# Optimization experiments

Measured on AMD Instinct MI355X. Metric: run time of the kernel, lower is better.

## Reference

```python
import jax, jax.numpy as jnp
import numpy as np

N = 50000      # nodes
E = 800000     # edges (before self-loops)
HD = 256       # hidden_dim
H = 4          # heads
C = 64         # per-head channels (hidden_dim // 4)
L = 3          # num_layers
G = 512        # graphs in batch
NEG = 0.2      # LeakyReLU negative slope
EPS = 1e-5     # BatchNorm eps


def setup_inputs() -> dict:
    key = jax.random.key(0)
    ks = jax.random.split(key, 16)
    s_in = 1.0 / np.sqrt(HD)
    inp = {
        "x": jax.random.normal(ks[0], (N, 9), dtype=jnp.float32),
        "edge_index": jax.random.randint(ks[1], (2, E), 0, N, dtype=jnp.int64),
        "edge_attr": jax.random.normal(ks[2], (E, 5), dtype=jnp.float32),
        "batch": jnp.sort(jax.random.randint(ks[3], (N,), 0, G, dtype=jnp.int64)),
        # embeddings
        "Wn": jax.random.normal(ks[4], (9, HD), dtype=jnp.float32) / 3.0,
        "bn_b": jnp.zeros((HD,), jnp.float32),
        "We": jax.random.normal(ks[5], (5, HD), dtype=jnp.float32) / 2.3,
        "be_b": jnp.zeros((HD,), jnp.float32),
        # per-layer GATConv params (stacked over L)
        "lin_w": jax.random.normal(ks[6], (L, HD, H * C), dtype=jnp.float32) * s_in,
        "att_src": jax.random.normal(ks[7], (L, H, C), dtype=jnp.float32) * s_in,
        "att_dst": jax.random.normal(ks[8], (L, H, C), dtype=jnp.float32) * s_in,
        "lin_edge_w": jax.random.normal(ks[9], (L, HD, H * C), dtype=jnp.float32) * s_in,
        "att_edge": jax.random.normal(ks[10], (L, H, C), dtype=jnp.float32) * s_in,
        "conv_bias": jnp.zeros((L, H * C), jnp.float32),
        # BatchNorm affine params (eval mode: running_mean=0, running_var=1)
        "gamma": jnp.ones((L, HD), jnp.float32),
        "beta": jnp.zeros((L, HD), jnp.float32),
    }
    return inp


def _segment_softmax(logits, seg, num):
    m = jax.ops.segment_max(logits, seg, num_segments=num)
    m = jnp.where(jnp.isfinite(m), m, 0.0)
    e = jnp.exp(logits - m[seg])
    s = jax.ops.segment_sum(e, seg, num_segments=num)
    return e / (s[seg] + 1e-16)


def _gat_layer(x, row, col, edge_attr, lin_w, att_s, att_d, lin_e_w, att_e, bias):
    # add self-loops; self-loop edge_attr = mean of incoming edge_attr (PyG fill_value='mean')
    deg = jax.ops.segment_sum(jnp.ones((row.shape[0],), x.dtype), col, num_segments=N)
    loop_attr = jax.ops.segment_sum(edge_attr, col, num_segments=N) / jnp.maximum(deg, 1.0)[:, None]
    sl = jnp.arange(N, dtype=row.dtype)
    r = jnp.concatenate([row, sl])
    c = jnp.concatenate([col, sl])
    ea = jnp.concatenate([edge_attr, loop_attr], axis=0)  # [E+N, HD]

    xh = (x @ lin_w).reshape(N, H, C)                     # [N,H,C]
    a_src = jnp.einsum('nhc,hc->nh', xh, att_s)           # [N,H]
    a_dst = jnp.einsum('nhc,hc->nh', xh, att_d)
    eh = (ea @ lin_e_w).reshape(-1, H, C)                 # [E+N,H,C]
    a_e = jnp.einsum('ehc,hc->eh', eh, att_e)

    alpha = a_src[r] + a_dst[c] + a_e                     # [E+N,H]
    alpha = jnp.where(alpha >= 0, alpha, NEG * alpha)     # leaky_relu
    alpha = _segment_softmax(alpha, c, N)

    msg = xh[r] * alpha[:, :, None]                       # gather + weight
    out = jax.ops.segment_sum(msg, c, num_segments=N)     # scatter-add
    return out.reshape(N, H * C) + bias


def reference(x, edge_index, edge_attr, batch, Wn, bn_b, We, be_b,
              lin_w, att_src, att_dst, lin_edge_w, att_edge, conv_bias,
              gamma, beta):
    row, col = edge_index[0], edge_index[1]
    h = x @ Wn + bn_b                     # node embedding [N,HD]
    ea = edge_attr @ We + be_b            # edge embedding [E,HD]
    inv_std = 1.0 / jnp.sqrt(1.0 + EPS)   # BN eval, running stats (0,1)
    for l in range(L):
        h = _gat_layer(h, row, col, ea, lin_w[l], att_src[l], att_dst[l],
                       lin_edge_w[l], att_edge[l], conv_bias[l])
        h = h * inv_std * gamma[l] + beta[l]
        h = jax.nn.relu(h)                # dropout = identity (eval)
    # global mean pool over graphs
    cnt = jax.ops.segment_sum(jnp.ones((N,), h.dtype), batch, num_segments=G)
    pooled = jax.ops.segment_sum(h, batch, num_segments=G) / jnp.maximum(cnt, 1.0)[:, None]
    return pooled
```

## Files before the change

### kernel.cpp

```cpp
#include <hip/hip_runtime.h>
#include <hip/hip_fp16.h>
#include <math.h>

#define HD 256
#define NHEAD 4
#define CH 64
#define NLAYER 3
#define NEG_SLOPE 0.2f

typedef __attribute__((ext_vector_type(8))) _Float16 half8;
typedef __attribute__((ext_vector_type(4))) _Float16 half4v;
typedef __attribute__((ext_vector_type(4))) float float4v;
typedef __attribute__((ext_vector_type(4))) unsigned uint4v;

__global__ __launch_bounds__(256) void embed_count_kernel(
    const float* __restrict__ x, const float* __restrict__ Wn,
    const float* __restrict__ bn_b, _Float16* __restrict__ h, int N,
    const int* __restrict__ col, int* __restrict__ deg, int E,
    int embedBlocks) {
  int tid = threadIdx.x;
  if ((int)blockIdx.x < embedBlocks) {
    int base = blockIdx.x * 8;
    __shared__ float xs[8][9];
    int nn = N - base;
    if (nn > 8) nn = 8;
    if (tid < nn * 9) xs[tid / 9][tid % 9] = x[(size_t)base * 9 + tid];
    __syncthreads();
    float b = bn_b[tid];
    for (int i = 0; i < nn; ++i) {
      float v = b;
#pragma unroll
      for (int k = 0; k < 9; ++k) v += xs[i][k] * Wn[k * HD + tid];
      h[(size_t)(base + i) * HD + tid] = (_Float16)v;
    }
  } else {
    int e = (blockIdx.x - embedBlocks) * 256 + tid;
    if (e < E) atomicAdd(&deg[col[e]], 1);
  }
}

__global__ __launch_bounds__(256) void wc_bfrag_kernel(
    const float* __restrict__ lin_edge_w, const float* __restrict__ att_edge,
    const float* __restrict__ We, const float* __restrict__ be_b,
    float* __restrict__ Wc, float* __restrict__ bc,
    const float* __restrict__ lin_w, _Float16* __restrict__ Bf_hi) {
  int tid = threadIdx.x;
  if (blockIdx.x < 12) {
    int lh = blockIdx.x;
    int l = lh >> 2, hh = lh & 3;
    __shared__ float weff[256];
    int j = tid;
    const float* lw = lin_edge_w + (size_t)l * HD * HD + (size_t)j * HD + hh * CH;
    const float* ae = att_edge + l * HD + hh * CH;
    float s = 0.f;
#pragma unroll 8
    for (int c = 0; c < CH; ++c) s += lw[c] * ae[c];
    weff[j] = s;
    __syncthreads();
    if (j < 5) {
      float acc = 0.f;
      for (int t = 0; t < 256; ++t) acc += We[j * HD + t] * weff[t];
      Wc[j * 12 + lh] = acc;
    } else if (j == 5) {
      float acc = 0.f;
      for (int t = 0; t < 256; ++t) acc += be_b[t] * weff[t];
      bc[lh] = acc;
    }
  } else {
    int bid = (blockIdx.x - 12) * 4 + (tid >> 6);
    int l = bid >> 7;
    int kt = (bid >> 4) & 7, ntg = bid & 15;
    int lane = tid & 63;
    const float* B = lin_w + (size_t)l * HD * HD;
    size_t base = ((size_t)bid * 64 + lane) * 8;
    int k0 = kt * 32 + (lane >> 4) * 8;
    int n = ((ntg >= 8) ? 128 : 0) + (lane & 15) * 8 + (ntg & 7);
#pragma unroll
    for (int j = 0; j < 8; ++j) {
      Bf_hi[base + j] = (_Float16)B[(size_t)(k0 + j) * HD + n];
    }
  }
}

__global__ __launch_bounds__(256) void tile_sums_kernel(
    const int* __restrict__ deg, int* __restrict__ tsum, int N) {
  __shared__ int red[256];
  int i = blockIdx.x * 256 + threadIdx.x;
  red[threadIdx.x] = (i < N) ? deg[i] : 0;
  __syncthreads();
  for (int off = 128; off > 0; off >>= 1) {
    if (threadIdx.x < off) red[threadIdx.x] += red[threadIdx.x + off];
    __syncthreads();
  }
  if (threadIdx.x == 0) tsum[blockIdx.x] = red[0];
}

__global__ __launch_bounds__(64) void scan_tsums_kernel(
    const int* __restrict__ tsum, int* __restrict__ toff, int T) {
  int lane = threadIdx.x;
  int carry = 0;
  for (int base = 0; base < T; base += 64) {
    int i = base + lane;
    int orig = (i < T) ? tsum[i] : 0;
    int v = orig;
#pragma unroll
    for (int off = 1; off < 64; off <<= 1) {
      int t = __shfl_up(v, off, 64);
      if (lane >= off) v += t;
    }
    if (i < T) toff[i] = carry + v - orig;
    carry += __shfl(v, 63, 64);
  }
}

__global__ __launch_bounds__(256) void scan_local_kernel(
    const int* __restrict__ deg, const int* __restrict__ toff,
    int* __restrict__ row_start, int N, int E) {
  __shared__ int buf[256];
  int i = blockIdx.x * 256 + threadIdx.x;
  int v = (i < N) ? deg[i] : 0;
  buf[threadIdx.x] = v;
  __syncthreads();
  for (int off = 1; off < 256; off <<= 1) {
    int t = (threadIdx.x >= off) ? buf[threadIdx.x - off] : 0;
    __syncthreads();
    buf[threadIdx.x] += t;
    __syncthreads();
  }
  if (i < N) row_start[i] = toff[blockIdx.x] + buf[threadIdx.x] - v;
  if (blockIdx.x == 0 && threadIdx.x == 0) row_start[N] = E;
}

__global__ __launch_bounds__(256) void scatter_csr_ae_kernel(
    const int* __restrict__ row, const int* __restrict__ col,
    const float* __restrict__ edge_attr, const int* __restrict__ row_start,
    int* __restrict__ cursor, const float* __restrict__ Wc,
    const float* __restrict__ bc, unsigned* __restrict__ ecsr, int E) {
  __shared__ float sWc[60];
  __shared__ float sbc[12];
  int t = threadIdx.x;
  if (t < 60) sWc[t] = Wc[t];
  if (t < 12) sbc[t] = bc[t];
  __syncthreads();
  int e = blockIdx.x * 256 + t;
  if (e >= E) return;
  int c = col[e];
  int p = atomicAdd(&cursor[c], 1);
  float ea[5];
#pragma unroll
  for (int k = 0; k < 5; ++k) ea[k] = edge_attr[(size_t)e * 5 + k];
  unsigned rec[8];
  rec[0] = (unsigned)row[e];
#pragma unroll
  for (int l = 0; l < NLAYER; ++l) {
    float av[NHEAD];
#pragma unroll
    for (int hh = 0; hh < NHEAD; ++hh) {
      int lh = l * NHEAD + hh;
      float s = sbc[lh];
#pragma unroll
      for (int k = 0; k < 5; ++k) s += ea[k] * sWc[k * 12 + lh];
      av[hh] = s;
    }
    __half2 p0 = __floats2half2_rn(av[0], av[1]);
    __half2 p1 = __floats2half2_rn(av[2], av[3]);
    rec[1 + 2 * l] = *(unsigned*)&p0;
    rec[2 + 2 * l] = *(unsigned*)&p1;
  }
  rec[7] = 0u;
  int slot = row_start[c] + p;
  uint4v* dst = (uint4v*)(ecsr + (size_t)slot * 8);
  uint4v v0 = {rec[0], rec[1], rec[2], rec[3]};
  uint4v v1 = {rec[4], rec[5], rec[6], rec[7]};
  dst[0] = v0;
  dst[1] = v1;
}

__global__ __launch_bounds__(512) void mfma_gemm_fused_kernel(
    const _Float16* __restrict__ A, const _Float16* __restrict__ Bf_hi,
    const float* __restrict__ att_s, const float* __restrict__ att_d,
    __half* __restrict__ xh_h, float* __restrict__ a_src,
    float* __restrict__ a_dst, int N) {
  __shared__ _Float16 sBh[4096];
  const int tid = threadIdx.x;
  const int wave = tid >> 6, lane = tid & 63;
  const int m = lane & 15, quad = lane >> 4;
  const int y = blockIdx.y;
  const int rowbase = blockIdx.x * 128 + wave * 16;
  const int arow = rowbase + m;
  const int arowc = (arow < N) ? arow : (N - 1);

  float4v acc[8];
#pragma unroll
  for (int nt = 0; nt < 8; ++nt) acc[nt] = (float4v){0.f, 0.f, 0.f, 0.f};

  for (int kt = 0; kt < 8; ++kt) {
    __syncthreads();
    {
      const float4* gh = (const float4*)(Bf_hi + ((size_t)kt * 16 + y * 8) * 512);
      ((float4*)sBh)[tid] = gh[tid];
    }
    half8 a = *(const half8*)(A + (size_t)arowc * HD + kt * 32 + quad * 8);
    __syncthreads();
#pragma unroll
    for (int nt = 0; nt < 8; ++nt) {
      half8 bhi = *(const half8*)&sBh[nt * 512 + lane * 8];
      acc[nt] = __builtin_amdgcn_mfma_f32_16x16x32_f16(a, bhi, acc[nt], 0, 0, 0);
    }
  }

  const int hh = y * 2 + (m >> 3);
  const int colbase = y * 128 + m * 8;
  float ats[8], atd[8];
#pragma unroll
  for (int nt = 0; nt < 8; ++nt) {
    ats[nt] = att_s[colbase + nt];
    atd[nt] = att_d[colbase + nt];
  }
  _Float16* xf = (_Float16*)xh_h;
#pragma unroll
  for (int r = 0; r < 4; ++r) {
    int orow = rowbase + quad * 4 + r;
    bool valid = orow < N;
    float ps = 0.f, pd = 0.f;
    half8 h0;
#pragma unroll
    for (int nt = 0; nt < 8; ++nt) {
      h0[nt] = (_Float16)acc[nt][r];
      ps += acc[nt][r] * ats[nt];
      pd += acc[nt][r] * atd[nt];
    }
    if (valid) {
      *(half8*)(xf + (size_t)orow * HD + colbase) = h0;
    }
    ps += __shfl_xor(ps, 1, 64);
    ps += __shfl_xor(ps, 2, 64);
    ps += __shfl_xor(ps, 4, 64);
    pd += __shfl_xor(pd, 1, 64);
    pd += __shfl_xor(pd, 2, 64);
    pd += __shfl_xor(pd, 4, 64);
    if (valid && (m & 7) == 0) {
      a_src[(size_t)orow * NHEAD + hh] = ps;
      a_dst[(size_t)orow * NHEAD + hh] = pd;
    }
  }
}

__global__ __launch_bounds__(256) void fused_aggregate_kernel(
    const __half* __restrict__ xh_h, const unsigned* __restrict__ ecsr,
    const int* __restrict__ row_start, int lsel,
    const float* __restrict__ a_src, const float* __restrict__ a_dst,
    const float* __restrict__ cb, const float* __restrict__ gm,
    const float* __restrict__ bt, float inv_std, _Float16* __restrict__ hout,
    int N) {
  int tid = threadIdx.x;
  int n = blockIdx.x * 4 + (tid >> 6);
  if (n >= N) return;
  int lane = tid & 63;
  int s = row_start[n], e = row_start[n + 1];

  const int hw = lane >> 4;
  const int eidx = lane & 15;
  const int t = lane;
  const int ch = t * 4;
  const half4v* xh4 = (const half4v*)xh_h;
  const float based = a_dst[n * 4 + hw];
  const int aofs = 1 + 2 * lsel + (hw >> 1);
  const bool hi_half = (hw & 1);

  float a0 = 0.f, a1 = 0.f, a2 = 0.f, a3 = 0.f;
  float zpart = 0.f, aepart = 0.f;

  const int base_src = lane & 48;
  for (int chunk = s; chunk < e; chunk += 16) {
    int myedge = chunk + eidx;
    int r_my = 0;
    float w_my = 0.f;
    if (myedge < e) {
      const unsigned* rp = ecsr + (size_t)myedge * 8;
      r_my = (int)rp[0];
      unsigned aw = rp[aofs];
      __half2 h2 = *(__half2*)&aw;
      float ae = hi_half ? __high2float(h2) : __low2float(h2);
      float lg = a_src[r_my * 4 + hw] + based + ae;
      lg = (lg >= 0.f) ? lg : NEG_SLOPE * lg;
      w_my = __expf(lg);
      zpart += w_my;
      aepart += ae;
    }
#pragma unroll
    for (int u = 0; u < 16; ++u) {
      float w = __shfl(w_my, base_src + u, 64);
      int ru = __shfl(r_my, base_src + u, 64);
      half4v xv = xh4[(size_t)ru * 64 + t];
      a0 += w * (float)xv[0];
      a1 += w * (float)xv[1];
      a2 += w * (float)xv[2];
      a3 += w * (float)xv[3];
    }
  }
#pragma unroll
  for (int off = 1; off < 16; off <<= 1) {
    zpart += __shfl_xor(zpart, off, 64);
    aepart += __shfl_xor(aepart, off, 64);
  }
  float dinv = (e > s) ? 1.0f / (float)(e - s) : 1.0f;
  float sl = a_src[n * 4 + hw] + based + aepart * dinv;
  sl = (sl >= 0.f) ? sl : NEG_SLOPE * sl;
  float wself = __expf(sl);
  half4v sv = xh4[(size_t)n * 64 + t];
  a0 += wself * (float)sv[0];
  a1 += wself * (float)sv[1];
  a2 += wself * (float)sv[2];
  a3 += wself * (float)sv[3];
  float zinv = 1.0f / (zpart + wself + 1e-16f);

  half4v ho;
  ho[0] = (_Float16)fmaxf((a0 * zinv + cb[ch + 0]) * inv_std * gm[ch + 0] + bt[ch + 0], 0.f);
  ho[1] = (_Float16)fmaxf((a1 * zinv + cb[ch + 1]) * inv_std * gm[ch + 1] + bt[ch + 1], 0.f);
  ho[2] = (_Float16)fmaxf((a2 * zinv + cb[ch + 2]) * inv_std * gm[ch + 2] + bt[ch + 2], 0.f);
  ho[3] = (_Float16)fmaxf((a3 * zinv + cb[ch + 3]) * inv_std * gm[ch + 3] + bt[ch + 3], 0.f);
  *(half4v*)&hout[(size_t)n * HD + ch] = ho;
}

__global__ __launch_bounds__(128) void pool_kernel(
    const _Float16* __restrict__ h, const int* __restrict__ batch,
    float* __restrict__ out, int N) {
  int g = blockIdx.x;
  int ch = blockIdx.y * 128 + threadIdx.x;
  __shared__ int s_lo, s_hi;
  if (threadIdx.x == 0) {
    int lo = 0, hi = N;
    while (lo < hi) { int mid = (lo + hi) >> 1; if (batch[mid] < g) lo = mid + 1; else hi = mid; }
    s_lo = lo;
    lo = 0; hi = N;
    while (lo < hi) { int mid = (lo + hi) >> 1; if (batch[mid] < g + 1) lo = mid + 1; else hi = mid; }
    s_hi = lo;
  }
  __syncthreads();
  int lo = s_lo, hi = s_hi;
  float acc = 0.f;
  for (int n = lo; n < hi; ++n) acc += (float)h[(size_t)n * HD + ch];
  int cnt = hi - lo;
  out[(size_t)g * HD + ch] = acc / (float)(cnt > 0 ? cnt : 1);
}

extern "C" void kernel_launch(void* const* d_in, const int* in_sizes, int n_in,
                              void* d_out, int out_size, void* d_ws, size_t ws_size,
                              hipStream_t stream) {
  const float* x = (const float*)d_in[0];
  const int* ei = (const int*)d_in[1];
  const float* edge_attr = (const float*)d_in[2];
  const int* batch = (const int*)d_in[3];
  const float* Wn = (const float*)d_in[4];
  const float* bn_b = (const float*)d_in[5];
  const float* We = (const float*)d_in[6];
  const float* be_b = (const float*)d_in[7];
  const float* lin_w = (const float*)d_in[8];
  const float* att_src = (const float*)d_in[9];
  const float* att_dst = (const float*)d_in[10];
  const float* lin_edge_w = (const float*)d_in[11];
  const float* att_edge = (const float*)d_in[12];
  const float* conv_bias = (const float*)d_in[13];
  const float* gamma = (const float*)d_in[14];
  const float* beta = (const float*)d_in[15];

  const int N = in_sizes[3];
  const int E = in_sizes[1] / 2;
  const int G = out_size / HD;
  const int* row = ei;
  const int* col = ei + E;

  char* ws = (char*)d_ws;
  size_t off = 0;
  auto alloc = [&](size_t bytes) -> char* {
    char* p = ws + off;
    off += (bytes + 255) & ~(size_t)255;
    return p;
  };
  _Float16* h = (_Float16*)alloc((size_t)N * HD * 2);
  __half* xh_h = (__half*)alloc((size_t)N * HD * 2);
  float* a_src = (float*)alloc((size_t)N * NHEAD * 4);
  float* a_dst = (float*)alloc((size_t)N * NHEAD * 4);
  unsigned* ecsr = (unsigned*)alloc((size_t)E * 32);
  int* deg = (int*)alloc((size_t)N * 4);
  int* row_start = (int*)alloc((size_t)(N + 1) * 4);
  int* cursor = (int*)alloc((size_t)N * 4);
  int* tsum = (int*)alloc(4096);
  int* toff = (int*)alloc(4096);
  float* Wc = (float*)alloc(64 * 4);
  float* bc = (float*)alloc(16 * 4);
  _Float16* Bf_hi = (_Float16*)alloc((size_t)NLAYER * HD * HD * 2);

  (void)hipMemsetAsync(deg, 0, (size_t)N * 4, stream);
  (void)hipMemsetAsync(cursor, 0, (size_t)N * 4, stream);

  int embedBlocks = (N + 7) / 8;
  int countBlocks = (E + 255) / 256;
  embed_count_kernel<<<embedBlocks + countBlocks, 256, 0, stream>>>(
      x, Wn, bn_b, h, N, col, deg, E, embedBlocks);
  wc_bfrag_kernel<<<12 + NLAYER * 32, 256, 0, stream>>>(
      lin_edge_w, att_edge, We, be_b, Wc, bc, lin_w, Bf_hi);
  int T = (N + 255) / 256;
  tile_sums_kernel<<<T, 256, 0, stream>>>(deg, tsum, N);
  scan_tsums_kernel<<<1, 64, 0, stream>>>(tsum, toff, T);
  scan_local_kernel<<<T, 256, 0, stream>>>(deg, toff, row_start, N, E);
  scatter_csr_ae_kernel<<<(E + 255) / 256, 256, 0, stream>>>(
      row, col, edge_attr, row_start, cursor, Wc, bc, ecsr, E);

  const float inv_std = 1.0f / sqrtf(1.0f + 1e-5f);
  for (int l = 0; l < NLAYER; ++l) {
    dim3 gg((N + 127) / 128, 2);
    mfma_gemm_fused_kernel<<<gg, 512, 0, stream>>>(
        h, Bf_hi + (size_t)l * HD * HD,
        att_src + l * HD, att_dst + l * HD, xh_h, a_src, a_dst, N);
    fused_aggregate_kernel<<<(N + 3) / 4, 256, 0, stream>>>(
        xh_h, ecsr, row_start, l, a_src, a_dst,
        conv_bias + l * HD, gamma + l * HD, beta + l * HD, inv_std, h, N);
  }
  dim3 pg(G, 2);
  pool_kernel<<<pg, 128, 0, stream>>>(h, batch, (float*)d_out, N);
}
```

Before: 515.2 us.

## Batch neighbor gathers ahead of softmax, grid-stride aggregate, vectorize pooling

The aggregation kernel now issues all 16 neighbor feature-row gathers for a chunk before computing the attention weights. This raises memory-level parallelism instead of interleaving one load per shuffle and FMA. It also becomes a persistent grid-stride loop capped at 2560 blocks, with the bias/BatchNorm affine folded into per-thread constants hoisted out of the node loop. The pooling kernel drops the second grid dimension and reads half2 pairs with four independent accumulators. The costs are higher register pressure from holding 16 half4 values, and possible load imbalance with fewer blocks.

```diff
diff --git a/kernel.cpp b/kernel.cpp
--- a/kernel.cpp
+++ b/kernel.cpp
@@ -253,83 +253,106 @@
     const float* __restrict__ cb, const float* __restrict__ gm,
     const float* __restrict__ bt, float inv_std, _Float16* __restrict__ hout,
     int N) {
-  int tid = threadIdx.x;
-  int n = blockIdx.x * 4 + (tid >> 6);
-  if (n >= N) return;
-  int lane = tid & 63;
-  int s = row_start[n], e = row_start[n + 1];
-
+  const int tid = threadIdx.x;
+  const int lane = tid & 63;
   const int hw = lane >> 4;
   const int eidx = lane & 15;
   const int t = lane;
   const int ch = t * 4;
-  const half4v* xh4 = (const half4v*)xh_h;
-  const float based = a_dst[n * 4 + hw];
+  const char* __restrict__ xb = (const char*)xh_h;
+  const char* __restrict__ eb = (const char*)ecsr;
+  const char* __restrict__ ab = (const char*)a_src;
   const int aofs = 1 + 2 * lsel + (hw >> 1);
   const bool hi_half = (hw & 1);
-
-  float a0 = 0.f, a1 = 0.f, a2 = 0.f, a3 = 0.f;
-  float zpart = 0.f, aepart = 0.f;
-
   const int base_src = lane & 48;
-  for (int chunk = s; chunk < e; chunk += 16) {
-    int myedge = chunk + eidx;
-    int r_my = 0;
-    float w_my = 0.f;
-    if (myedge < e) {
-      const unsigned* rp = ecsr + (size_t)myedge * 8;
-      r_my = (int)rp[0];
-      unsigned aw = rp[aofs];
-      __half2 h2 = *(__half2*)&aw;
-      float ae = hi_half ? __high2float(h2) : __low2float(h2);
-      float lg = a_src[r_my * 4 + hw] + based + ae;
-      lg = (lg >= 0.f) ? lg : NEG_SLOPE * lg;
-      w_my = __expf(lg);
+
+  const float gs0 = gm[ch + 0] * inv_std, gs1 = gm[ch + 1] * inv_std;
+  const float gs2 = gm[ch + 2] * inv_std, gs3 = gm[ch + 3] * inv_std;
+  const float of0 = cb[ch + 0] * gs0 + bt[ch + 0];
+  const float of1 = cb[ch + 1] * gs1 + bt[ch + 1];
+  const float of2 = cb[ch + 2] * gs2 + bt[ch + 2];
+  const float of3 = cb[ch + 3] * gs3 + bt[ch + 3];
+
+  const int stride = gridDim.x * 4;
+  for (int n = blockIdx.x * 4 + (tid >> 6); n < N; n += stride) {
+    int s = row_start[n], e = row_start[n + 1];
+    half4v sv = *(const half4v*)(xb + ((unsigned)n << 9) + ((unsigned)t << 3));
+    float based = a_dst[(size_t)n * 4 + hw];
+
+    float a0 = 0.f, a1 = 0.f, a2 = 0.f, a3 = 0.f;
+    float zpart = 0.f, aepart = 0.f;
+
+    for (int chunk = s; chunk < e; chunk += 16) {
+      int myedge = chunk + eidx;
+      bool mev = myedge < e;
+      int r_my = 0;
+      unsigned aw_u = 0;
+      if (mev) {
+        const unsigned* rp = (const unsigned*)(eb + ((unsigned)myedge << 5));
+        r_my = (int)rp[0];
+        aw_u = rp[aofs];
+      }
+      int ru[16];
+#pragma unroll
+      for (int u = 0; u < 16; ++u) ru[u] = __shfl(r_my, base_src + u, 64);
+      half4v xv[16];
+#pragma unroll
+      for (int u = 0; u < 16; ++u)
+        xv[u] = *(const half4v*)(xb + ((unsigned)ru[u] << 9) + ((unsigned)t << 3));
+
+      float w_my = 0.f, ae = 0.f;
+      if (mev) {
+        __half2 h2 = *(__half2*)&aw_u;
+        ae = hi_half ? __high2float(h2) : __low2float(h2);
+        float lg = *(const float*)(ab + ((unsigned)r_my << 4) + ((unsigned)hw << 2))
+                   + based + ae;
+        lg = (lg >= 0.f) ? lg : NEG_SLOPE * lg;
+        w_my = __expf(lg);
+      }
       zpart += w_my;
       aepart += ae;
-    }
-#pragma unroll
-    for (int u = 0; u < 16; ++u) {
-      float w = __shfl(w_my, base_src + u, 64);
-      int ru = __shfl(r_my, base_src + u, 64);
-      half4v xv = xh4[(size_t)ru * 64 + t];
-      a0 += w * (float)xv[0];
-      a1 += w * (float)xv[1];
-      a2 += w * (float)xv[2];
-      a3 += w * (float)xv[3];
-    }
-  }
-#pragma unroll
-  for (int off = 1; off < 16; off <<= 1) {
-    zpart += __shfl_xor(zpart, off, 64);
-    aepart += __shfl_xor(aepart, off, 64);
-  }
-  float dinv = (e > s) ? 1.0f / (float)(e - s) : 1.0f;
-  float sl = a_src[n * 4 + hw] + based + aepart * dinv;
-  sl = (sl >= 0.f) ? sl : NEG_SLOPE * sl;
-  float wself = __expf(sl);
-  half4v sv = xh4[(size_t)n * 64 + t];
-  a0 += wself * (float)sv[0];
-  a1 += wself * (float)sv[1];
-  a2 += wself * (float)sv[2];
-  a3 += wself * (float)sv[3];
-  float zinv = 1.0f / (zpart + wself + 1e-16f);
-
-  half4v ho;
-  ho[0] = (_Float16)fmaxf((a0 * zinv + cb[ch + 0]) * inv_std * gm[ch + 0] + bt[ch + 0], 0.f);
-  ho[1] = (_Float16)fmaxf((a1 * zinv + cb[ch + 1]) * inv_std * gm[ch + 1] + bt[ch + 1], 0.f);
-  ho[2] = (_Float16)fmaxf((a2 * zinv + cb[ch + 2]) * inv_std * gm[ch + 2] + bt[ch + 2], 0.f);
-  ho[3] = (_Float16)fmaxf((a3 * zinv + cb[ch + 3]) * inv_std * gm[ch + 3] + bt[ch + 3], 0.f);
-  *(half4v*)&hout[(size_t)n * HD + ch] = ho;
+
+#pragma unroll
+      for (int u = 0; u < 16; ++u) {
+        float w = __shfl(w_my, base_src + u, 64);
+        a0 += w * (float)xv[u][0];
+        a1 += w * (float)xv[u][1];
+        a2 += w * (float)xv[u][2];
+        a3 += w * (float)xv[u][3];
+      }
+    }
+#pragma unroll
+    for (int off = 1; off < 16; off <<= 1) {
+      zpart += __shfl_xor(zpart, off, 64);
+      aepart += __shfl_xor(aepart, off, 64);
+    }
+    float dinv = (e > s) ? 1.0f / (float)(e - s) : 1.0f;
+    float sl = *(const float*)(ab + ((unsigned)n << 4) + ((unsigned)hw << 2))
+               + based + aepart * dinv;
+    sl = (sl >= 0.f) ? sl : NEG_SLOPE * sl;
+    float wself = __expf(sl);
+    a0 += wself * (float)sv[0];
+    a1 += wself * (float)sv[1];
+    a2 += wself * (float)sv[2];
+    a3 += wself * (float)sv[3];
+    float zinv = 1.0f / (zpart + wself + 1e-16f);
+
+    half4v ho;
+    ho[0] = (_Float16)fmaxf(a0 * zinv * gs0 + of0, 0.f);
+    ho[1] = (_Float16)fmaxf(a1 * zinv * gs1 + of1, 0.f);
+    ho[2] = (_Float16)fmaxf(a2 * zinv * gs2 + of2, 0.f);
+    ho[3] = (_Float16)fmaxf(a3 * zinv * gs3 + of3, 0.f);
+    *(half4v*)&hout[(size_t)n * HD + ch] = ho;
+  }
 }
 
 __global__ __launch_bounds__(128) void pool_kernel(
     const _Float16* __restrict__ h, const int* __restrict__ batch,
     float* __restrict__ out, int N) {
   int g = blockIdx.x;
-  int ch = blockIdx.y * 128 + threadIdx.x;
+  int tid = threadIdx.x;
   __shared__ int s_lo, s_hi;
-  if (threadIdx.x == 0) {
+  if (tid == 0) {
     int lo = 0, hi = N;
     while (lo < hi) { int mid = (lo + hi) >> 1; if (batch[mid] < g) lo = mid + 1; else hi = mid; }
     s_lo = lo;
@@ -339,10 +362,32 @@
   }
   __syncthreads();
   int lo = s_lo, hi = s_hi;
-  float acc = 0.f;
-  for (int n = lo; n < hi; ++n) acc += (float)h[(size_t)n * HD + ch];
+  const __half2* h2 = (const __half2*)h;
+  float a0 = 0.f, b0 = 0.f, a1 = 0.f, b1 = 0.f;
+  float a2 = 0.f, b2 = 0.f, a3 = 0.f, b3 = 0.f;
+  int n = lo;
+  for (; n + 4 <= hi; n += 4) {
+    __half2 v0 = h2[(size_t)(n + 0) * 128 + tid];
+    __half2 v1 = h2[(size_t)(n + 1) * 128 + tid];
+    __half2 v2 = h2[(size_t)(n + 2) * 128 + tid];
+    __half2 v3 = h2[(size_t)(n + 3) * 128 + tid];
+    a0 += __low2float(v0); b0 += __high2float(v0);
+    a1 += __low2float(v1); b1 += __high2float(v1);
+    a2 += __low2float(v2); b2 += __high2float(v2);
+    a3 += __low2float(v3); b3 += __high2float(v3);
+  }
+  for (; n < hi; ++n) {
+    __half2 v = h2[(size_t)n * 128 + tid];
+    a0 += __low2float(v); b0 += __high2float(v);
+  }
+  float sa = (a0 + a1) + (a2 + a3);
+  float sb = (b0 + b1) + (b2 + b3);
   int cnt = hi - lo;
-  out[(size_t)g * HD + ch] = acc / (float)(cnt > 0 ? cnt : 1);
+  float inv = 1.0f / (float)(cnt > 0 ? cnt : 1);
+  float2 o;
+  o.x = sa * inv;
+  o.y = sb * inv;
+  *(float2*)&out[(size_t)g * HD + tid * 2] = o;
 }
 
 extern "C" void kernel_launch(void* const* d_in, const int* in_sizes, int n_in,
@@ -409,15 +454,16 @@
       row, col, edge_attr, row_start, cursor, Wc, bc, ecsr, E);
 
   const float inv_std = 1.0f / sqrtf(1.0f + 1e-5f);
+  int quads = (N + 3) / 4;
+  int aggBlocks = quads < 2560 ? quads : 2560;
   for (int l = 0; l < NLAYER; ++l) {
     dim3 gg((N + 127) / 128, 2);
     mfma_gemm_fused_kernel<<<gg, 512, 0, stream>>>(
         h, Bf_hi + (size_t)l * HD * HD,
         att_src + l * HD, att_dst + l * HD, xh_h, a_src, a_dst, N);
-    fused_aggregate_kernel<<<(N + 3) / 4, 256, 0, stream>>>(
+    fused_aggregate_kernel<<<aggBlocks, 256, 0, stream>>>(
         xh_h, ecsr, row_start, l, a_src, a_dst,
         conv_bias + l * HD, gamma + l * HD, beta + l * HD, inv_std, h, N);
   }
-  dim3 pg(G, 2);
-  pool_kernel<<<pg, 128, 0, stream>>>(h, batch, (float*)d_out, N);
-}
+  pool_kernel<<<G, 128, 0, stream>>>(h, batch, (float*)d_out, N);
+}
```

New measurement: 489.7 us. 5.0% less time.
